# Kernel optimization log

Measured on AMD Instinct MI355X. Metric: run time of the kernel, lower is better.

The kernel has to match this reference:

```python
import jax, jax.numpy as jnp
import numpy as np

D_MODEL = 1024
NUM_HEADS = 16
D_K = D_MODEL // NUM_HEADS
THETA = 10000.0
SEQ = 4096
BATCH = 1


def _rope(x, pos):
    # x: [..., S, d_k]; pos: [S]
    inv_freq = 1.0 / (THETA ** (jnp.arange(0, D_K, 2, dtype=jnp.float32) / D_K))  # [d_k/2]
    freqs = pos.astype(jnp.float32)[:, None] * inv_freq[None, :]  # [S, d_k/2]
    cos = jnp.cos(freqs)
    sin = jnp.sin(freqs)
    x_even = x[..., ::2]
    x_odd = x[..., 1::2]
    out1 = cos * x_even - sin * x_odd
    out2 = sin * x_even + cos * x_odd
    # interleave: stack on new last axis then flatten (matches torch.stack(...,-1).flatten(-2))
    out = jnp.stack([out1, out2], axis=-1).reshape(x.shape)
    return out


def setup_inputs() -> dict:
    key = jax.random.key(0)
    ks = jax.random.split(key, 5)
    std = (2.0 / (D_MODEL + D_MODEL)) ** 0.5
    x = jax.random.normal(ks[0], (BATCH, SEQ, D_MODEL), dtype=jnp.float32)
    wq = jax.random.normal(ks[1], (D_MODEL, D_MODEL), dtype=jnp.float32) * std
    wk = jax.random.normal(ks[2], (D_MODEL, D_MODEL), dtype=jnp.float32) * std
    wv = jax.random.normal(ks[3], (D_MODEL, D_MODEL), dtype=jnp.float32) * std
    wo = jax.random.normal(ks[4], (D_MODEL, D_MODEL), dtype=jnp.float32) * std
    return {"x": x, "wq": wq, "wk": wk, "wv": wv, "wo": wo}


def reference(x, wq, wk, wv, wo):
    b, s, d = x.shape
    # projections: y = x @ W.T  (weight stored [out, in])
    q = jnp.einsum('bsd,od->bso', x, wq)
    k = jnp.einsum('bsd,od->bso', x, wk)
    v = jnp.einsum('bsd,od->bso', x, wv)
    # split heads -> [b, h, s, d_k]
    q = q.reshape(b, s, NUM_HEADS, D_K).transpose(0, 2, 1, 3)
    k = k.reshape(b, s, NUM_HEADS, D_K).transpose(0, 2, 1, 3)
    v = v.reshape(b, s, NUM_HEADS, D_K).transpose(0, 2, 1, 3)
    pos = jnp.arange(s)
    q = _rope(q, pos)
    k = _rope(k, pos)
    scores = jnp.einsum('bhqd,bhkd->bhqk', q, k) / (D_K ** 0.5)
    causal = jnp.tril(jnp.ones((s, s), dtype=bool))
    scores = jnp.where(causal, scores, -jnp.inf)
    attn = jax.nn.softmax(scores, axis=-1)
    out = jnp.einsum('bhqk,bhkd->bhqd', attn, v)
    out = out.transpose(0, 2, 1, 3).reshape(b, s, d)
    out = jnp.einsum('bsd,od->bso', out, wo)
    return out
```

## Files before the change

### kernel.cpp

```cpp
#include <hip/hip_runtime.h>
#include <math.h>

#define SEQ    4096
#define DMODEL 1024
#define NHEADS 16
#define DK     64

typedef unsigned short u16;
typedef short bh8 __attribute__((ext_vector_type(8)));
typedef float f4  __attribute__((ext_vector_type(4)));
typedef float f16v __attribute__((ext_vector_type(16)));

__device__ __forceinline__ u16 f2b(float f) {
    union { float f; unsigned u; } v; v.f = f;
    unsigned u = v.u;
    return (u16)((u + 0x7FFFu + ((u >> 16) & 1u)) >> 16);
}
__device__ __forceinline__ unsigned bits_of(float f) {
    union { float f; unsigned u; } v; v.f = f; return v.u;
}
__device__ __forceinline__ unsigned pk2(float a, float b) {
#if __has_builtin(__builtin_amdgcn_perm)
    return __builtin_amdgcn_perm(bits_of(b), bits_of(a), 0x07060302u);
#else
    return (bits_of(a) >> 16) | (bits_of(b) & 0xFFFF0000u);
#endif
}
__device__ __forceinline__ float fexp2(float x) {
#if __has_builtin(__builtin_amdgcn_exp2f)
    return __builtin_amdgcn_exp2f(x);
#else
    return exp2f(x);
#endif
}
__device__ __forceinline__ float ffract(float x) {
#if __has_builtin(__builtin_amdgcn_fractf)
    return __builtin_amdgcn_fractf(x);
#else
    return x - floorf(x);
#endif
}

__global__ void cvt_all_kernel(const float* __restrict__ x,
                               const float* __restrict__ wq, const float* __restrict__ wk,
                               const float* __restrict__ wv, const float* __restrict__ wo,
                               u16* __restrict__ xb, u16* __restrict__ wb)
{
    const int NX = SEQ * DMODEL / 8;
    const int NW = DMODEL * DMODEL / 8;
    int i = blockIdx.x * blockDim.x + threadIdx.x;
    if (i >= NX + 4 * NW) return;
    const float* src; u16* dst; int j;
    if (i < NX) { src = x; dst = xb; j = i; }
    else {
        int k = i - NX;
        int wsel = k >> 17;
        j = k & (NW - 1);
        src = (wsel == 0) ? wq : (wsel == 1) ? wk : (wsel == 2) ? wv : wo;
        dst = wb + (size_t)wsel * DMODEL * DMODEL;
    }
    const float4* p = (const float4*)src + (size_t)j * 2;
    float4 a = p[0], b = p[1];
    __align__(16) u16 r[8] = { f2b(a.x), f2b(a.y), f2b(a.z), f2b(a.w),
                               f2b(b.x), f2b(b.y), f2b(b.z), f2b(b.w) };
    *(uint4*)(dst + (size_t)j * 8) = *(const uint4*)r;
}

template<int MODE>
__global__ __launch_bounds__(256) void gemm_bt(
    const u16* __restrict__ A, const u16* __restrict__ B,
    void* __restrict__ out, u16* __restrict__ Qh, u16* __restrict__ Kh,
    u16* __restrict__ Vt, int M, int N, int K)
{
    constexpr int BN  = (MODE == 0) ? 64 : 128;
    constexpr int NJ  = BN / 32;
    constexpr int ASZ = 128 * 32;
    constexpr int BSZ = BN * 32;

    __shared__ __align__(16) u16 sh[2][ASZ + BSZ];

    const int g    = blockIdx.x;
    const int xt   = (g >> 8) * 8 + (g & 7);
    const int yt   = (g & 255) >> 3;
    const int m0   = yt * 128, n0 = xt * BN;

    const int t    = threadIdx.x;
    const int w    = t >> 6, lane = t & 63;
    const int quad = lane >> 4, l16 = lane & 15;
    const int wm   = w >> 1,  wn  = w & 1;
    const int lr   = lane >> 2;
    const int lc   = (lane & 3) * 8;
    const int c0   = 2 * w, c1 = 2 * w + 1;

    f4 acc[4][NJ];
#pragma unroll
    for (int i = 0; i < 4; ++i)
#pragma unroll
        for (int j = 0; j < NJ; ++j) { f4 z = {0.f,0.f,0.f,0.f}; acc[i][j] = z; }

    const size_t aofs0 = (size_t)(m0 + c0 * 16 + lr) * K + lc;
    const size_t aofs1 = (size_t)(m0 + c1 * 16 + lr) * K + lc;
    size_t bofs0 = 0, bofs1 = 0;
    if (MODE == 0) {
        bofs0 = (size_t)(n0 + w * 16 + lr) * K + lc;
    } else {
        const int br0 = c0 * 16 + lr, br1 = c1 * 16 + lr;
        const int p0 = (br0 & 64) | ((br0 & 15) << 2) | ((br0 >> 4) & 3);
        const int p1 = (br1 & 64) | ((br1 & 15) << 2) | ((br1 >> 4) & 3);
        bofs0 = (size_t)(n0 + p0) * K + lc;
        bofs1 = (size_t)(n0 + p1) * K + lc;
    }

#define GLD(src_, dst_)                                                        \
    __builtin_amdgcn_global_load_lds(                                          \
        (const __attribute__((address_space(1))) unsigned int*)(src_),         \
        (__attribute__((address_space(3))) unsigned int*)(dst_), 16, 0, 0)

#define STAGE(buf_, k0_) do {                                                  \
    GLD(A + aofs0 + (k0_), &sh[buf_][c0 * 512]);                               \
    GLD(A + aofs1 + (k0_), &sh[buf_][c1 * 512]);                               \
    if (MODE == 0) {                                                           \
        GLD(B + bofs0 + (k0_), &sh[buf_][ASZ + w * 512]);                      \
    } else {                                                                   \
        GLD(B + bofs0 + (k0_), &sh[buf_][ASZ + c0 * 512]);                     \
        GLD(B + bofs1 + (k0_), &sh[buf_][ASZ + c1 * 512]);                     \
    }                                                                          \
} while (0)

    STAGE(0, 0);
    __syncthreads();

    int b = 0;
    for (int k0 = 0; k0 < K; k0 += 32) {
        if (k0 + 32 < K) STAGE(b ^ 1, k0 + 32);

        const u16* As_ = &sh[b][0];
        const u16* Bs_ = &sh[b][ASZ];
        bh8 af[4], bf_[NJ];
#pragma unroll
        for (int i = 0; i < 4; ++i)
            af[i] = *(const bh8*)&As_[(wm * 64 + i * 16 + l16) * 32 + quad * 8];
#pragma unroll
        for (int j = 0; j < NJ; ++j)
            bf_[j] = *(const bh8*)&Bs_[(wn * (BN / 2) + j * 16 + l16) * 32 + quad * 8];
#pragma unroll
        for (int i = 0; i < 4; ++i)
#pragma unroll
            for (int j = 0; j < NJ; ++j)
                acc[i][j] = __builtin_amdgcn_mfma_f32_16x16x32_bf16(af[i], bf_[j], acc[i][j], 0, 0, 0);
        __syncthreads();
        b ^= 1;
    }

    if (MODE == 0) {
#pragma unroll
        for (int i = 0; i < 4; ++i) {
            const int row = m0 + wm * 64 + i * 16 + quad * 4;
#pragma unroll
            for (int j = 0; j < NJ; ++j) {
                const int col = n0 + wn * (BN / 2) + j * 16 + l16;
#pragma unroll
                for (int r = 0; r < 4; ++r)
                    ((float*)out)[(size_t)(row + r) * N + col] = acc[i][j][r];
            }
        }
    } else {
        const int sect = n0 >> 10;
        if (sect < 2) {
            const int hh = ((n0 & 1023) + wn * 64) >> 6;
            u16* dst = (sect == 0) ? Qh : Kh;
            const float qscl = (sect == 0) ? 0.18033688011112042f : 1.0f;
            const int dbase = l16 * 4;
            const float invfA = exp2f((float)(dbase)     * (-13.287712379549449f / 64.0f))
                                * 0.15915494309189535f;
            const float invfB = exp2f((float)(dbase + 2) * (-13.287712379549449f / 64.0f))
                                * 0.15915494309189535f;
#pragma unroll
            for (int i = 0; i < 4; ++i) {
                const int srow0 = m0 + wm * 64 + i * 16 + quad * 4;
#pragma unroll
                for (int r = 0; r < 4; ++r) {
                    const int srow = srow0 + r;
                    const float revA = ffract((float)srow * invfA);
                    const float revB = ffract((float)srow * invfB);
                    const float snA = __builtin_amdgcn_sinf(revA);
                    const float csA = __builtin_amdgcn_cosf(revA);
                    const float snB = __builtin_amdgcn_sinf(revB);
                    const float csB = __builtin_amdgcn_cosf(revB);
                    const float e0 = acc[i][0][r], o0 = acc[i][1][r];
                    const float e1 = acc[i][2][r], o1 = acc[i][3][r];
                    const float v0 = (csA * e0 - snA * o0) * qscl;
                    const float v1 = (snA * e0 + csA * o0) * qscl;
                    const float v2 = (csB * e1 - snB * o1) * qscl;
                    const float v3 = (snB * e1 + csB * o1) * qscl;
                    uint2 st;
                    st.x = (unsigned)f2b(v0) | ((unsigned)f2b(v1) << 16);
                    st.y = (unsigned)f2b(v2) | ((unsigned)f2b(v3) << 16);
                    *(uint2*)&dst[((size_t)hh * SEQ + srow) * DK + dbase] = st;
                }
            }
        } else {
            u16* scr = &sh[0][0];
            const int cfb = wn * 64 + l16 * 4;
            const int xv  = (l16 & 7) << 2;
            __syncthreads();
#pragma unroll
            for (int i = 0; i < 4; ++i) {
                const int s0 = wm * 64 + i * 16 + quad * 4;
                const int s8 = s0 >> 2;
#pragma unroll
                for (int j = 0; j < NJ; ++j) {
                    __align__(8) u16 pk[4];
#pragma unroll
                    for (int r = 0; r < 4; ++r) pk[r] = f2b(acc[i][j][r]);
                    *(unsigned long long*)&scr[(cfb + j) * 128 + (s8 ^ xv) * 4] =
                        *(const unsigned long long*)pk;
                }
            }
            __syncthreads();
            const int hh0 = (n0 & 1023) >> 6;
            const int sl  = t & 15;
#pragma unroll
            for (int jj = 0; jj < 8; ++jj) {
                const int cfull = jj * 16 + (t >> 4);
                const int hd    = hh0 + (cfull >> 6);
                const int dd    = cfull & 63;
                const int rxv   = ((cfull >> 2) & 7) << 2;
                bh8 vv = *(const bh8*)&scr[cfull * 128 + ((sl * 2) ^ rxv) * 4];
                *(bh8*)&Vt[((size_t)hd * DK + dd) * SEQ + m0 + sl * 8] = vv;
            }
        }
    }
#undef STAGE
#undef GLD
}

__global__ __launch_bounds__(512, 4) void attn_mfma_kernel(
    const u16* __restrict__ Qh, const u16* __restrict__ Kh,
    const u16* __restrict__ Vt, u16* __restrict__ ctx)
{
    __shared__ __align__(16) u16 smem[2][16384];

    const int id   = blockIdx.x;
    const int head = (id & 7) + 8 * ((id >> 3) & 1);
    const int bx   = id >> 4;

    const int t    = threadIdx.x;
    const int w    = t >> 6, lane = t & 63;
    const int qb   = w & 1, kb = w >> 1;
    const int l31  = lane & 31, hl = lane >> 5;
    const int r7   = l31 & 7;

    const u16* Kbase = Kh + (size_t)head * SEQ * DK;
    const u16* Vbase = Vt + (size_t)head * DK * SEQ;

    int kread[4];
#pragma unroll
    for (int c = 0; c < 4; ++c)
        kread[c] = (kb * 32 + l31) * 64 + (((c * 2 + hl) ^ r7) * 8);
    int vread[2][2];
#pragma unroll
    for (int db = 0; db < 2; ++db)
#pragma unroll
        for (int kc = 0; kc < 2; ++kc)
            vread[db][kc] = (db * 32 + l31) * 128
                          + (((kb * 4 + kc * 2 + hl) ^ r7) * 8);

    int koff[2], voff[2];
#pragma unroll
    for (int i = 0; i < 2; ++i) {
        const int krow = i * 64 + (t >> 3);
        koff[i] = krow * DK + (((t & 7) ^ (krow & 7)) * 8);
        const int vdr  = i * 32 + (t >> 4);
        voff[i] = vdr * SEQ + (((t & 15) ^ (vdr & 7)) * 8);
    }
    const int dstK = w * 512;
    const int dstV = 8192 + w * 512;

    const f16v z16 = {0,0,0,0,0,0,0,0,0,0,0,0,0,0,0,0};

#define STAGE(buf_, kbase_) do {                                               \
    _Pragma("unroll")                                                          \
    for (int i_ = 0; i_ < 2; ++i_) {                                           \
        __builtin_amdgcn_global_load_lds(                                      \
            (const __attribute__((address_space(1))) unsigned int*)            \
                (Kbase + (size_t)(kbase_) * DK + koff[i_]),                    \
            (__attribute__((address_space(3))) unsigned int*)                  \
                &smem[buf_][i_ * 4096 + dstK], 16, 0, 0);                      \
        __builtin_amdgcn_global_load_lds(                                      \
            (const __attribute__((address_space(1))) unsigned int*)            \
                (Vbase + (kbase_) + voff[i_]),                                 \
            (__attribute__((address_space(3))) unsigned int*)                  \
                &smem[buf_][i_ * 4096 + dstV], 16, 0, 0);                      \
    }                                                                          \
} while (0)

    for (int part = 0; part < 2; ++part) {
        const int qt = part ? (63 - bx) : bx;
        const int q0 = qt * 64;
        const int nt = qt / 2 + 1;
        const int qg = q0 + qb * 32 + l31;

        bh8 qa[4];
        {
            const u16* qrow = Qh + ((size_t)head * SEQ + qg) * DK;
#pragma unroll
            for (int c = 0; c < 4; ++c)
                qa[c] = *(const bh8*)(qrow + c * 16 + hl * 8);
        }

        f16v o0 = z16;
        f16v o1 = z16;
        float lsum = 0.f;

        __syncthreads();
        STAGE(0, 0);
        __syncthreads();

        int b = 0;
        for (int kt = 0; kt < nt; ++kt) {
            const bool have_next = (kt + 1 < nt);
            if (have_next) STAGE(b ^ 1, (kt + 1) * 128);

            const int  kbase = kt * 128;
            const bool diag  = (kt == nt - 1);
            const bool skip  = diag && (kbase + kb * 32 > q0 + qb * 32 + 31);

            if (!skip) {
                __builtin_amdgcn_s_setprio(1);
                bh8 kf0 = *(const bh8*)&smem[b][kread[0]];
                f16v s = __builtin_amdgcn_mfma_f32_32x32x16_bf16(kf0, qa[0], z16, 0, 0, 0);
#pragma unroll
                for (int c = 1; c < 4; ++c) {
                    bh8 kf = *(const bh8*)&smem[b][kread[c]];
                    s = __builtin_amdgcn_mfma_f32_32x32x16_bf16(kf, qa[c], s, 0, 0, 0);
                }
                __builtin_amdgcn_s_setprio(0);
                if (diag) {
#pragma unroll
                    for (int r = 0; r < 16; ++r) {
                        const int keyg = kbase + kb * 32 + (r & 3) + 8 * (r >> 2) + 4 * hl;
                        if (keyg > qg) s[r] = -1.0e30f;
                    }
                }
                float p[16];
#pragma unroll
                for (int r = 0; r < 16; ++r) { p[r] = fexp2(s[r]); lsum += p[r]; }

#pragma unroll
                for (int kc = 0; kc < 2; ++kc) {
                    unsigned A0 = pk2(p[kc*8+0], p[kc*8+1]);
                    unsigned A1 = pk2(p[kc*8+2], p[kc*8+3]);
                    unsigned A2 = pk2(p[kc*8+4], p[kc*8+5]);
                    unsigned A3 = pk2(p[kc*8+6], p[kc*8+7]);
                    asm volatile("v_permlane32_swap_b32 %0, %1" : "+v"(A0), "+v"(A2));
                    asm volatile("v_permlane32_swap_b32 %0, %1" : "+v"(A1), "+v"(A3));
                    union { unsigned u[4]; bh8 v; } pb;
                    pb.u[0] = A0; pb.u[1] = A1; pb.u[2] = A2; pb.u[3] = A3;
                    bh8 va0 = *(const bh8*)&smem[b][8192 + vread[0][kc]];
                    bh8 va1 = *(const bh8*)&smem[b][8192 + vread[1][kc]];
                    __builtin_amdgcn_s_setprio(1);
                    o0 = __builtin_amdgcn_mfma_f32_32x32x16_bf16(va0, pb.v, o0, 0, 0, 0);
                    o1 = __builtin_amdgcn_mfma_f32_32x32x16_bf16(va1, pb.v, o1, 0, 0, 0);
                    __builtin_amdgcn_s_setprio(0);
                }
            }

            if (have_next) { __syncthreads(); b ^= 1; }
        }

        lsum += __shfl_xor(lsum, 32);
        __syncthreads();
        float* scr = (float*)&smem[0][0];
        union { f16v v; f4 q[4]; } uo0, uo1;
        uo0.v = o0; uo1.v = o1;
        if (kb != 0) {
            float* rec = scr + (((kb - 1) * 2 + qb) * 64 + lane) * 36;
#pragma unroll
            for (int j = 0; j < 4; ++j) {
                *(f4*)(rec + j * 4)      = uo0.q[j];
                *(f4*)(rec + 16 + j * 4) = uo1.q[j];
            }
            rec[32] = lsum;
        }
        __syncthreads();
        if (kb == 0) {
#pragma unroll
            for (int jr = 0; jr < 3; ++jr) {
                const float* rec = scr + ((jr * 2 + qb) * 64 + lane) * 36;
#pragma unroll
                for (int j = 0; j < 4; ++j) {
                    f4 a = *(const f4*)(rec + j * 4);
                    f4 c = *(const f4*)(rec + 16 + j * 4);
#pragma unroll
                    for (int e = 0; e < 4; ++e) {
                        uo0.q[j][e] += a[e];
                        uo1.q[j][e] += c[e];
                    }
                }
                lsum += rec[32];
            }
            const float linv = 1.f / lsum;
            const size_t rowbase = (size_t)qg * DMODEL + head * DK;
#pragma unroll
            for (int a = 0; a < 4; ++a) {
                unsigned lo = pk2(0.f, uo0.q[a][0] * linv) >> 16 |
                              (pk2(0.f, uo0.q[a][1] * linv) & 0xFFFF0000u);
                lo = (unsigned)f2b(uo0.q[a][0] * linv) | ((unsigned)f2b(uo0.q[a][1] * linv) << 16);
                unsigned hi = (unsigned)f2b(uo0.q[a][2] * linv) | ((unsigned)f2b(uo0.q[a][3] * linv) << 16);
                uint2 pkd; pkd.x = lo; pkd.y = hi;
                *(uint2*)&ctx[rowbase + a * 8 + 4 * hl] = pkd;
                lo = (unsigned)f2b(uo1.q[a][0] * linv) | ((unsigned)f2b(uo1.q[a][1] * linv) << 16);
                hi = (unsigned)f2b(uo1.q[a][2] * linv) | ((unsigned)f2b(uo1.q[a][3] * linv) << 16);
                pkd.x = lo; pkd.y = hi;
                *(uint2*)&ctx[rowbase + 32 + a * 8 + 4 * hl] = pkd;
            }
        }
    }
#undef STAGE
}

extern "C" void kernel_launch(void* const* d_in, const int* in_sizes, int n_in,
                              void* d_out, int out_size, void* d_ws, size_t ws_size,
                              hipStream_t stream)
{
    const float* x  = (const float*)d_in[0];
    const float* wq = (const float*)d_in[1];
    const float* wk = (const float*)d_in[2];
    const float* wv = (const float*)d_in[3];
    const float* wo = (const float*)d_in[4];
    float* out = (float*)d_out;

    char* ws = (char*)d_ws;
    const size_t MB = 1u << 20;
    u16* xb   = (u16*)(ws);
    u16* wqkv = (u16*)(ws + 8  * MB);
    u16* wob  = (u16*)(ws + 14 * MB);
    u16* Qh   = (u16*)(ws + 16 * MB);
    u16* Kh   = (u16*)(ws + 24 * MB);
    u16* Vtb  = (u16*)(ws + 32 * MB);
    u16* ctxb = (u16*)(ws + 40 * MB);

    const int NCVT = SEQ * DMODEL / 8 + 4 * (DMODEL * DMODEL / 8);
    cvt_all_kernel<<<NCVT / 256, 256, 0, stream>>>(x, wq, wk, wv, wo, xb, wqkv);

    gemm_bt<2><<<dim3(768), 256, 0, stream>>>(xb, wqkv, nullptr, Qh, Kh, Vtb,
                                              SEQ, 3 * DMODEL, DMODEL);

    attn_mfma_kernel<<<dim3(512), 512, 0, stream>>>(Qh, Kh, Vtb, ctxb);

    gemm_bt<0><<<dim3(512), 256, 0, stream>>>(ctxb, wob, out, nullptr, nullptr, nullptr,
                                              SEQ, DMODEL, DMODEL);
}
```

Baseline: 182.1 us.

## Restructure attention into one q-tile per block with split K/V staging

The attention kernel now runs one query tile per block (1024 blocks, heaviest tiles first) instead of pairing two tiles per block. K is double-buffered while V gets a single buffer that is loaded during the QK^T/softmax phase, with manual vmcnt waits and raw barriers, and LDS use is cut so occupancy can rise to 6 blocks per CU. The cross-warp reduction scratch now stores partial outputs as bf16 rather than fp32, which slightly reduces precision. The GEMM tile mapping moves from a swizzled 1D grid to a plain 2D grid, which may give up L2 locality.

```diff
diff --git a/kernel.cpp b/kernel.cpp
--- a/kernel.cpp
+++ b/kernel.cpp
@@ -18,6 +18,9 @@
 }
 __device__ __forceinline__ unsigned bits_of(float f) {
     union { float f; unsigned u; } v; v.f = f; return v.u;
+}
+__device__ __forceinline__ float u2f(unsigned u) {
+    union { unsigned u; float f; } v; v.u = u; return v.f;
 }
 __device__ __forceinline__ unsigned pk2(float a, float b) {
 #if __has_builtin(__builtin_amdgcn_perm)
@@ -79,15 +82,11 @@
 
     __shared__ __align__(16) u16 sh[2][ASZ + BSZ];
 
-    const int g    = blockIdx.x;
-    const int xt   = (g >> 8) * 8 + (g & 7);
-    const int yt   = (g & 255) >> 3;
-    const int m0   = yt * 128, n0 = xt * BN;
-
     const int t    = threadIdx.x;
     const int w    = t >> 6, lane = t & 63;
     const int quad = lane >> 4, l16 = lane & 15;
     const int wm   = w >> 1,  wn  = w & 1;
+    const int m0   = blockIdx.y * 128, n0 = blockIdx.x * BN;
     const int lr   = lane >> 2;
     const int lc   = (lane & 3) * 8;
     const int c0   = 2 * w, c1 = 2 * w + 1;
@@ -235,15 +234,16 @@
 #undef GLD
 }
 
-__global__ __launch_bounds__(512, 4) void attn_mfma_kernel(
+__global__ __launch_bounds__(512, 6) void attn_mfma_kernel(
     const u16* __restrict__ Qh, const u16* __restrict__ Kh,
     const u16* __restrict__ Vt, u16* __restrict__ ctx)
 {
-    __shared__ __align__(16) u16 smem[2][16384];
+    __shared__ __align__(16) u16 Ks[2][8192];
+    __shared__ __align__(16) u16 Vs[8192];
 
     const int id   = blockIdx.x;
     const int head = (id & 7) + 8 * ((id >> 3) & 1);
-    const int bx   = id >> 4;
+    const int qt   = 63 - (id >> 4);
 
     const int t    = threadIdx.x;
     const int w    = t >> 6, lane = t & 63;
@@ -274,150 +274,160 @@
         const int vdr  = i * 32 + (t >> 4);
         voff[i] = vdr * SEQ + (((t & 15) ^ (vdr & 7)) * 8);
     }
-    const int dstK = w * 512;
-    const int dstV = 8192 + w * 512;
+    const int dstKV = w * 512;
 
     const f16v z16 = {0,0,0,0,0,0,0,0,0,0,0,0,0,0,0,0};
 
-#define STAGE(buf_, kbase_) do {                                               \
+#define STAGE_K(buf_, kt_) do {                                                \
     _Pragma("unroll")                                                          \
-    for (int i_ = 0; i_ < 2; ++i_) {                                           \
+    for (int i_ = 0; i_ < 2; ++i_)                                             \
         __builtin_amdgcn_global_load_lds(                                      \
             (const __attribute__((address_space(1))) unsigned int*)            \
-                (Kbase + (size_t)(kbase_) * DK + koff[i_]),                    \
+                (Kbase + (size_t)(kt_) * 128 * DK + koff[i_]),                 \
             (__attribute__((address_space(3))) unsigned int*)                  \
-                &smem[buf_][i_ * 4096 + dstK], 16, 0, 0);                      \
+                &Ks[buf_][i_ * 4096 + dstKV], 16, 0, 0);                       \
+} while (0)
+
+#define STAGE_V(kt_) do {                                                      \
+    _Pragma("unroll")                                                          \
+    for (int i_ = 0; i_ < 2; ++i_)                                             \
         __builtin_amdgcn_global_load_lds(                                      \
             (const __attribute__((address_space(1))) unsigned int*)            \
-                (Vbase + (kbase_) + voff[i_]),                                 \
+                (Vbase + (kt_) * 128 + voff[i_]),                              \
             (__attribute__((address_space(3))) unsigned int*)                  \
-                &smem[buf_][i_ * 4096 + dstV], 16, 0, 0);                      \
-    }                                                                          \
+                &Vs[i_ * 4096 + dstKV], 16, 0, 0);                             \
 } while (0)
 
-    for (int part = 0; part < 2; ++part) {
-        const int qt = part ? (63 - bx) : bx;
-        const int q0 = qt * 64;
-        const int nt = qt / 2 + 1;
-        const int qg = q0 + qb * 32 + l31;
-
-        bh8 qa[4];
-        {
-            const u16* qrow = Qh + ((size_t)head * SEQ + qg) * DK;
-#pragma unroll
-            for (int c = 0; c < 4; ++c)
-                qa[c] = *(const bh8*)(qrow + c * 16 + hl * 8);
-        }
-
-        f16v o0 = z16;
-        f16v o1 = z16;
-        float lsum = 0.f;
-
-        __syncthreads();
-        STAGE(0, 0);
-        __syncthreads();
-
-        int b = 0;
-        for (int kt = 0; kt < nt; ++kt) {
-            const bool have_next = (kt + 1 < nt);
-            if (have_next) STAGE(b ^ 1, (kt + 1) * 128);
-
-            const int  kbase = kt * 128;
-            const bool diag  = (kt == nt - 1);
-            const bool skip  = diag && (kbase + kb * 32 > q0 + qb * 32 + 31);
-
-            if (!skip) {
+    const int q0 = qt * 64;
+    const int nt = qt / 2 + 1;
+    const int qg = q0 + qb * 32 + l31;
+
+    bh8 qa[4];
+    {
+        const u16* qrow = Qh + ((size_t)head * SEQ + qg) * DK;
+#pragma unroll
+        for (int c = 0; c < 4; ++c)
+            qa[c] = *(const bh8*)(qrow + c * 16 + hl * 8);
+    }
+
+    f16v o0 = z16;
+    f16v o1 = z16;
+    float lsum = 0.f;
+
+    STAGE_K(0, 0);
+
+    int b = 0;
+    for (int kt = 0; kt < nt; ++kt) {
+        __builtin_amdgcn_sched_barrier(0);
+        asm volatile("s_waitcnt vmcnt(0)" ::: "memory");
+        __builtin_amdgcn_s_barrier();
+        __builtin_amdgcn_sched_barrier(0);
+
+        STAGE_V(kt);
+        if (kt + 1 < nt) STAGE_K(b ^ 1, kt + 1);
+
+        const int  kbase = kt * 128;
+        const bool diag  = (kt == nt - 1);
+        const bool skip  = diag && (kbase + kb * 32 > q0 + qb * 32 + 31);
+
+        float p[16];
+        if (!skip) {
+            __builtin_amdgcn_s_setprio(1);
+            bh8 kf0 = *(const bh8*)&Ks[b][kread[0]];
+            f16v s = __builtin_amdgcn_mfma_f32_32x32x16_bf16(kf0, qa[0], z16, 0, 0, 0);
+#pragma unroll
+            for (int c = 1; c < 4; ++c) {
+                bh8 kf = *(const bh8*)&Ks[b][kread[c]];
+                s = __builtin_amdgcn_mfma_f32_32x32x16_bf16(kf, qa[c], s, 0, 0, 0);
+            }
+            __builtin_amdgcn_s_setprio(0);
+            if (diag) {
+#pragma unroll
+                for (int r = 0; r < 16; ++r) {
+                    const int keyg = kbase + kb * 32 + (r & 3) + 8 * (r >> 2) + 4 * hl;
+                    if (keyg > qg) s[r] = -1.0e30f;
+                }
+            }
+#pragma unroll
+            for (int r = 0; r < 16; ++r) { p[r] = fexp2(s[r]); lsum += p[r]; }
+        }
+
+        __builtin_amdgcn_sched_barrier(0);
+        if (kt + 1 < nt) asm volatile("s_waitcnt vmcnt(2)" ::: "memory");
+        else             asm volatile("s_waitcnt vmcnt(0)" ::: "memory");
+        __builtin_amdgcn_s_barrier();
+        __builtin_amdgcn_sched_barrier(0);
+
+        if (!skip) {
+#pragma unroll
+            for (int kc = 0; kc < 2; ++kc) {
+                unsigned A0 = pk2(p[kc*8+0], p[kc*8+1]);
+                unsigned A1 = pk2(p[kc*8+2], p[kc*8+3]);
+                unsigned A2 = pk2(p[kc*8+4], p[kc*8+5]);
+                unsigned A3 = pk2(p[kc*8+6], p[kc*8+7]);
+                asm volatile("v_permlane32_swap_b32 %0, %1" : "+v"(A0), "+v"(A2));
+                asm volatile("v_permlane32_swap_b32 %0, %1" : "+v"(A1), "+v"(A3));
+                union { unsigned u[4]; bh8 v; } pb;
+                pb.u[0] = A0; pb.u[1] = A1; pb.u[2] = A2; pb.u[3] = A3;
+                bh8 va0 = *(const bh8*)&Vs[vread[0][kc]];
+                bh8 va1 = *(const bh8*)&Vs[vread[1][kc]];
                 __builtin_amdgcn_s_setprio(1);
-                bh8 kf0 = *(const bh8*)&smem[b][kread[0]];
-                f16v s = __builtin_amdgcn_mfma_f32_32x32x16_bf16(kf0, qa[0], z16, 0, 0, 0);
-#pragma unroll
-                for (int c = 1; c < 4; ++c) {
-                    bh8 kf = *(const bh8*)&smem[b][kread[c]];
-                    s = __builtin_amdgcn_mfma_f32_32x32x16_bf16(kf, qa[c], s, 0, 0, 0);
-                }
+                o0 = __builtin_amdgcn_mfma_f32_32x32x16_bf16(va0, pb.v, o0, 0, 0, 0);
+                o1 = __builtin_amdgcn_mfma_f32_32x32x16_bf16(va1, pb.v, o1, 0, 0, 0);
                 __builtin_amdgcn_s_setprio(0);
-                if (diag) {
-#pragma unroll
-                    for (int r = 0; r < 16; ++r) {
-                        const int keyg = kbase + kb * 32 + (r & 3) + 8 * (r >> 2) + 4 * hl;
-                        if (keyg > qg) s[r] = -1.0e30f;
-                    }
-                }
-                float p[16];
-#pragma unroll
-                for (int r = 0; r < 16; ++r) { p[r] = fexp2(s[r]); lsum += p[r]; }
-
-#pragma unroll
-                for (int kc = 0; kc < 2; ++kc) {
-                    unsigned A0 = pk2(p[kc*8+0], p[kc*8+1]);
-                    unsigned A1 = pk2(p[kc*8+2], p[kc*8+3]);
-                    unsigned A2 = pk2(p[kc*8+4], p[kc*8+5]);
-                    unsigned A3 = pk2(p[kc*8+6], p[kc*8+7]);
-                    asm volatile("v_permlane32_swap_b32 %0, %1" : "+v"(A0), "+v"(A2));
-                    asm volatile("v_permlane32_swap_b32 %0, %1" : "+v"(A1), "+v"(A3));
-                    union { unsigned u[4]; bh8 v; } pb;
-                    pb.u[0] = A0; pb.u[1] = A1; pb.u[2] = A2; pb.u[3] = A3;
-                    bh8 va0 = *(const bh8*)&smem[b][8192 + vread[0][kc]];
-                    bh8 va1 = *(const bh8*)&smem[b][8192 + vread[1][kc]];
-                    __builtin_amdgcn_s_setprio(1);
-                    o0 = __builtin_amdgcn_mfma_f32_32x32x16_bf16(va0, pb.v, o0, 0, 0, 0);
-                    o1 = __builtin_amdgcn_mfma_f32_32x32x16_bf16(va1, pb.v, o1, 0, 0, 0);
-                    __builtin_amdgcn_s_setprio(0);
-                }
-            }
-
-            if (have_next) { __syncthreads(); b ^= 1; }
-        }
-
-        lsum += __shfl_xor(lsum, 32);
-        __syncthreads();
-        float* scr = (float*)&smem[0][0];
-        union { f16v v; f4 q[4]; } uo0, uo1;
-        uo0.v = o0; uo1.v = o1;
-        if (kb != 0) {
-            float* rec = scr + (((kb - 1) * 2 + qb) * 64 + lane) * 36;
+            }
+        }
+        b ^= 1;
+    }
+
+    lsum += __shfl_xor(lsum, 32);
+    __syncthreads();
+    unsigned* scru = (unsigned*)&Ks[0][0];
+    union { f16v v; f4 q[4]; } uo0, uo1;
+    uo0.v = o0; uo1.v = o1;
+    if (kb != 0) {
+        unsigned* rec = scru + (((kb - 1) * 2 + qb) * 64 + lane) * 20;
+#pragma unroll
+        for (int j = 0; j < 4; ++j) {
+            rec[j*2]     = (unsigned)f2b(uo0.q[j][0]) | ((unsigned)f2b(uo0.q[j][1]) << 16);
+            rec[j*2 + 1] = (unsigned)f2b(uo0.q[j][2]) | ((unsigned)f2b(uo0.q[j][3]) << 16);
+            rec[8 + j*2]     = (unsigned)f2b(uo1.q[j][0]) | ((unsigned)f2b(uo1.q[j][1]) << 16);
+            rec[8 + j*2 + 1] = (unsigned)f2b(uo1.q[j][2]) | ((unsigned)f2b(uo1.q[j][3]) << 16);
+        }
+        ((float*)rec)[16] = lsum;
+    }
+    __syncthreads();
+    if (kb == 0) {
+#pragma unroll
+        for (int jr = 0; jr < 3; ++jr) {
+            const unsigned* rec = scru + ((jr * 2 + qb) * 64 + lane) * 20;
 #pragma unroll
             for (int j = 0; j < 4; ++j) {
-                *(f4*)(rec + j * 4)      = uo0.q[j];
-                *(f4*)(rec + 16 + j * 4) = uo1.q[j];
-            }
-            rec[32] = lsum;
-        }
-        __syncthreads();
-        if (kb == 0) {
-#pragma unroll
-            for (int jr = 0; jr < 3; ++jr) {
-                const float* rec = scr + ((jr * 2 + qb) * 64 + lane) * 36;
-#pragma unroll
-                for (int j = 0; j < 4; ++j) {
-                    f4 a = *(const f4*)(rec + j * 4);
-                    f4 c = *(const f4*)(rec + 16 + j * 4);
-#pragma unroll
-                    for (int e = 0; e < 4; ++e) {
-                        uo0.q[j][e] += a[e];
-                        uo1.q[j][e] += c[e];
-                    }
-                }
-                lsum += rec[32];
-            }
-            const float linv = 1.f / lsum;
-            const size_t rowbase = (size_t)qg * DMODEL + head * DK;
-#pragma unroll
-            for (int a = 0; a < 4; ++a) {
-                unsigned lo = pk2(0.f, uo0.q[a][0] * linv) >> 16 |
-                              (pk2(0.f, uo0.q[a][1] * linv) & 0xFFFF0000u);
-                lo = (unsigned)f2b(uo0.q[a][0] * linv) | ((unsigned)f2b(uo0.q[a][1] * linv) << 16);
-                unsigned hi = (unsigned)f2b(uo0.q[a][2] * linv) | ((unsigned)f2b(uo0.q[a][3] * linv) << 16);
-                uint2 pkd; pkd.x = lo; pkd.y = hi;
-                *(uint2*)&ctx[rowbase + a * 8 + 4 * hl] = pkd;
-                lo = (unsigned)f2b(uo1.q[a][0] * linv) | ((unsigned)f2b(uo1.q[a][1] * linv) << 16);
-                hi = (unsigned)f2b(uo1.q[a][2] * linv) | ((unsigned)f2b(uo1.q[a][3] * linv) << 16);
-                pkd.x = lo; pkd.y = hi;
-                *(uint2*)&ctx[rowbase + 32 + a * 8 + 4 * hl] = pkd;
-            }
-        }
-    }
-#undef STAGE
+                const unsigned a0 = rec[j*2],     a1 = rec[j*2 + 1];
+                const unsigned c0 = rec[8 + j*2], c1 = rec[8 + j*2 + 1];
+                uo0.q[j][0] += u2f(a0 << 16);  uo0.q[j][1] += u2f(a0 & 0xFFFF0000u);
+                uo0.q[j][2] += u2f(a1 << 16);  uo0.q[j][3] += u2f(a1 & 0xFFFF0000u);
+                uo1.q[j][0] += u2f(c0 << 16);  uo1.q[j][1] += u2f(c0 & 0xFFFF0000u);
+                uo1.q[j][2] += u2f(c1 << 16);  uo1.q[j][3] += u2f(c1 & 0xFFFF0000u);
+            }
+            lsum += ((const float*)rec)[16];
+        }
+        const float linv = 1.f / lsum;
+        const size_t rowbase = (size_t)qg * DMODEL + head * DK;
+#pragma unroll
+        for (int a = 0; a < 4; ++a) {
+            unsigned lo = (unsigned)f2b(uo0.q[a][0] * linv) | ((unsigned)f2b(uo0.q[a][1] * linv) << 16);
+            unsigned hi = (unsigned)f2b(uo0.q[a][2] * linv) | ((unsigned)f2b(uo0.q[a][3] * linv) << 16);
+            uint2 pkd; pkd.x = lo; pkd.y = hi;
+            *(uint2*)&ctx[rowbase + a * 8 + 4 * hl] = pkd;
+            lo = (unsigned)f2b(uo1.q[a][0] * linv) | ((unsigned)f2b(uo1.q[a][1] * linv) << 16);
+            hi = (unsigned)f2b(uo1.q[a][2] * linv) | ((unsigned)f2b(uo1.q[a][3] * linv) << 16);
+            pkd.x = lo; pkd.y = hi;
+            *(uint2*)&ctx[rowbase + 32 + a * 8 + 4 * hl] = pkd;
+        }
+    }
+#undef STAGE_K
+#undef STAGE_V
 }
 
 extern "C" void kernel_launch(void* const* d_in, const int* in_sizes, int n_in,
@@ -444,11 +454,13 @@
     const int NCVT = SEQ * DMODEL / 8 + 4 * (DMODEL * DMODEL / 8);
     cvt_all_kernel<<<NCVT / 256, 256, 0, stream>>>(x, wq, wk, wv, wo, xb, wqkv);
 
-    gemm_bt<2><<<dim3(768), 256, 0, stream>>>(xb, wqkv, nullptr, Qh, Kh, Vtb,
-                                              SEQ, 3 * DMODEL, DMODEL);
-
-    attn_mfma_kernel<<<dim3(512), 512, 0, stream>>>(Qh, Kh, Vtb, ctxb);
-
-    gemm_bt<0><<<dim3(512), 256, 0, stream>>>(ctxb, wob, out, nullptr, nullptr, nullptr,
-                                              SEQ, DMODEL, DMODEL);
-}
+    dim3 gqkv(3 * DMODEL / 128, SEQ / 128);
+    gemm_bt<2><<<gqkv, 256, 0, stream>>>(xb, wqkv, nullptr, Qh, Kh, Vtb,
+                                         SEQ, 3 * DMODEL, DMODEL);
+
+    attn_mfma_kernel<<<dim3(1024), 512, 0, stream>>>(Qh, Kh, Vtb, ctxb);
+
+    dim3 go(DMODEL / 64, SEQ / 128);
+    gemm_bt<0><<<go, 256, 0, stream>>>(ctxb, wob, out, nullptr, nullptr, nullptr,
+                                       SEQ, DMODEL, DMODEL);
+}
```

Result: slower. 238.4 us (+30.9%).
